# Optimization experiments

Hardware: AMD Instinct MI355X
Metric: run time of the kernel (lower is better)

## Reference

```python
import jax, jax.numpy as jnp
import numpy as np

GROUP_SIZE = 128


def dequant_rtn(qweight, scale, zero_point):
    # qweight: [O, I] int, scale/zero_point: [O, I//GROUP_SIZE]
    O, I = qweight.shape
    G = scale.shape[1]
    gs = I // G
    q = qweight.reshape(O, G, gs).astype(jnp.float32)
    zp = zero_point.astype(jnp.float32)[:, :, None]
    w = (q - zp) * scale[:, :, None]
    return w.reshape(O, I)


def setup_inputs() -> dict:
    key = jax.random.key(0)
    k1, k2, k3, k4, k5 = jax.random.split(key, 5)
    B, S, I, O = 2, 2048, 4096, 11008
    G = I // GROUP_SIZE
    x = jax.random.normal(k1, (B, S, I), dtype=jnp.float32)
    qweight = jax.random.randint(k2, (O, I), 0, 16, dtype=jnp.int32)
    scale = jax.random.uniform(k3, (O, G), dtype=jnp.float32) * 0.02 + 1e-3
    zero_point = jax.random.randint(k4, (O, G), 0, 16, dtype=jnp.int32)
    bias = jax.random.normal(k5, (O,), dtype=jnp.float32)
    return {"x": x, "qweight": qweight, "scale": scale,
            "zero_point": zero_point, "bias": bias}


def reference(x, qweight, scale, zero_point, bias):
    # weight-only path: dequant weight, then F.linear(x, w, bias)
    w = dequant_rtn(qweight, scale, zero_point)  # [O, I] fp32
    return jnp.einsum('bsi,oi->bso', x, w) + bias
```

## Files before the change

### kernel.cpp

```cpp
#include <hip/hip_runtime.h>
#include <cstdint>
#include <cstddef>

typedef __attribute__((ext_vector_type(4))) int i32x4;
typedef __bf16 bf16;
typedef __attribute__((ext_vector_type(8))) __bf16 bf16x8;
typedef __attribute__((ext_vector_type(4))) float f32x4;

#define BM 128
#define BN 128
#define BKB 128
#define GROUP_M 16
#define GM256 4
#define NXCD 8

__device__ __forceinline__ unsigned bf16_rne(float f) {
  unsigned u = __float_as_uint(f);
  unsigned r = 0x7FFFu + ((u >> 16) & 1u);
  return ((u + r) >> 16) & 0xFFFFu;
}
__device__ __forceinline__ unsigned pack2(float a, float b) {
  return bf16_rne(a) | (bf16_rne(b) << 16);
}
__device__ __forceinline__ int pack4i8(int a, int b, int c, int d) {
  return (a & 0xFF) | ((b & 0xFF) << 8) | ((c & 0xFF) << 16) | (d << 24);
}
__device__ __forceinline__ int q_i8(float v) {
  v = fminf(fmaxf(v, -127.0f), 127.0f);
  return __float2int_rn(v);
}

__global__ __launch_bounds__(256) void prep_kernel(
    const float* __restrict__ x, char* __restrict__ xq, float* __restrict__ xscale,
    int M,
    const int* __restrict__ q, const float* __restrict__ scale,
    const int* __restrict__ zp, char* __restrict__ wq, float* __restrict__ wscale,
    int K, int G) {
  __shared__ float red[4];
  const int b = blockIdx.x;
  const int tid = threadIdx.x;
  float f[16];

  if (b < M) {
    const float4* src = (const float4*)(x + (size_t)b * K);
#pragma unroll
    for (int i = 0; i < 4; ++i) {
      float4 v = src[tid + 256 * i];
      f[4 * i + 0] = v.x; f[4 * i + 1] = v.y;
      f[4 * i + 2] = v.z; f[4 * i + 3] = v.w;
    }
  } else {
    const int row = b - M;
    const int4* src = (const int4*)(q + (size_t)row * K);
    const float* srow = scale + (size_t)row * G;
    const int*   zrow = zp + (size_t)row * G;
#pragma unroll
    for (int i = 0; i < 4; ++i) {
      const int j = tid + 256 * i;
      const int g = j >> 5;
      const float s = srow[g];
      const float nzs = -s * (float)zrow[g];
      int4 qv = src[j];
      f[4 * i + 0] = fmaf((float)qv.x, s, nzs);
      f[4 * i + 1] = fmaf((float)qv.y, s, nzs);
      f[4 * i + 2] = fmaf((float)qv.z, s, nzs);
      f[4 * i + 3] = fmaf((float)qv.w, s, nzs);
    }
  }

  float m = 0.f;
#pragma unroll
  for (int j = 0; j < 16; ++j) m = fmaxf(m, fabsf(f[j]));
#pragma unroll
  for (int off = 32; off >= 1; off >>= 1) m = fmaxf(m, __shfl_xor(m, off));
  if ((tid & 63) == 0) red[tid >> 6] = m;
  __syncthreads();
  m = fmaxf(fmaxf(red[0], red[1]), fmaxf(red[2], red[3]));

  const float inv = m > 0.f ? 127.0f / m : 0.f;
  int pk[4];
#pragma unroll
  for (int i = 0; i < 4; ++i)
    pk[i] = pack4i8(q_i8(f[4 * i + 0] * inv), q_i8(f[4 * i + 1] * inv),
                    q_i8(f[4 * i + 2] * inv), q_i8(f[4 * i + 3] * inv));

  char* dst = (b < M) ? (xq + (size_t)b * K) : (wq + (size_t)(b - M) * K);
  int* dst_i32 = (int*)dst;
#pragma unroll
  for (int i = 0; i < 4; ++i) dst_i32[tid + 256 * i] = pk[i];

  if (tid == 0) {
    if (b < M) xscale[b] = m * (1.0f / 127.0f);
    else       wscale[b - M] = m * (1.0f / 127.0f);
  }
}

typedef __attribute__((address_space(1))) void gas_void;
typedef __attribute__((address_space(3))) void las_void;

__device__ __forceinline__ void load_lds16(const void* g, void* l) {
  __builtin_amdgcn_global_load_lds((gas_void*)g, (las_void*)l, 16, 0, 0);
}


#define STAGE_A_H(buf, h, ktb) do {                                           \
    load_lds16(A + abase + (size_t)(ktb) + aoff0 + (size_t)(h) * 64 * K,      \
               &Al[buf][(h) * 8192 + dw]);                                    \
    load_lds16(A + abase + (size_t)(ktb) + aoff1 + (size_t)(h) * 64 * K,      \
               &Al[buf][16384 + (h) * 8192 + dw]);                            \
  } while (0)

#define STAGE_B_H(buf, h, ktb) do {                                           \
    load_lds16(Bw + bbase + (size_t)(ktb) + boff0 + (size_t)(h) * 32 * K,     \
               &Bl[buf][(h) * 16384 + dw]);                                   \
    load_lds16(Bw + bbase + (size_t)(ktb) + boff1 + (size_t)(h) * 32 * K,     \
               &Bl[buf][(h) * 16384 + 8192 + dw]);                            \
  } while (0)

__global__ __launch_bounds__(512, 2) void gemm_i8_256(
    const char* __restrict__ A,
    const char* __restrict__ Bw,
    const float* __restrict__ ascale,
    const float* __restrict__ bscale,
    const float* __restrict__ bias,
    float* __restrict__ C,
    int M, int N, int K) {
  __shared__ __align__(16) char Al[2][256 * 128];
  __shared__ __align__(16) char Bl[2][256 * 128];
  const int tid  = threadIdx.x;
  const int wave = tid >> 6;
  const int lane = tid & 63;
  const int quad = lane >> 4;
  const int l16  = lane & 15;
  const int wq3  = wave & 3;
  const int wmb  = (wave >> 2) * 128;
  const int wnb  = wq3 * 64;

  const int nbm = M / 256, nbn = N / 256;
  const int cpx = (nbm * nbn) / NXCD;
  const int swz = ((int)blockIdx.x % NXCD) * cpx + (int)blockIdx.x / NXCD;
  const int per_group = GM256 * nbn;
  const int gid = swz / per_group;
  const int rem = swz - gid * per_group;
  int gm = nbm - gid * GM256; if (gm > GM256) gm = GM256;
  const int bm = (gid * GM256 + (rem % gm)) * 256;
  const int bn = (rem / gm) * 256;

  const int r0 = tid >> 3;
  const int kq16 = (((tid & 7) ^ (r0 & 7)) * 16);
  const size_t aoff0 = (size_t)r0 * K + kq16;
  const size_t aoff1 = aoff0 + (size_t)128 * K;
  const size_t boff0 = (size_t)((r0 >> 5) * 64 + (r0 & 31)) * K + kq16;
  const size_t boff1 = boff0 + (size_t)128 * K;
  const int dw = wave * 1024;
  const size_t abase = (size_t)bm * K;
  const size_t bbase = (size_t)bn * K;
  const int NT = K / 128;

  i32x4 acc[8][4];
#pragma unroll
  for (int i = 0; i < 8; ++i)
#pragma unroll
    for (int j = 0; j < 4; ++j)
      acc[i][j] = (i32x4){0, 0, 0, 0};

  STAGE_A_H(0, 0, 0);
  STAGE_A_H(0, 1, 0);
  STAGE_B_H(0, 0, 0);
  STAGE_B_H(0, 1, 0);
  asm volatile("s_waitcnt vmcnt(0)" ::: "memory");
  __builtin_amdgcn_s_barrier();
  __builtin_amdgcn_sched_barrier(0);

  for (int t = 0; t < NT; ++t) {
    const int cur = t & 1;
    const int nxt = cur ^ 1;
    const int kt1 = (t + 1) * 128;

    if (t + 1 < NT) {
      STAGE_A_H(nxt, 0, kt1);
      STAGE_A_H(nxt, 1, kt1);
      STAGE_B_H(nxt, 0, kt1);
      STAGE_B_H(nxt, 1, kt1);
    }

#pragma unroll
    for (int ks = 0; ks < 2; ++ks) {
      i32x4 afr[8], bfr[4];
#pragma unroll
      for (int tm = 0; tm < 8; ++tm) {
        int row = wmb + tm * 16 + l16;
        int kq  = ks * 4 + quad;
        afr[tm] = *(const i32x4*)&Al[cur][(row * 8 + (kq ^ (row & 7))) * 16];
      }
#pragma unroll
      for (int j = 0; j < 4; ++j) {
        int p  = (j >> 1) * 128 + wq3 * 32 + (j & 1) * 16 + l16;
        int kq = ks * 4 + quad;
        bfr[j] = *(const i32x4*)&Bl[cur][(p * 8 + (kq ^ (p & 7))) * 16];
      }
#pragma unroll
      for (int tm = 0; tm < 8; ++tm)
#pragma unroll
        for (int j = 0; j < 4; ++j)
          acc[tm][j] = __builtin_amdgcn_mfma_i32_16x16x64_i8(
              afr[tm], bfr[j], acc[tm][j], 0, 0, 0);
    }

    asm volatile("s_waitcnt vmcnt(0)" ::: "memory");
    __builtin_amdgcn_s_barrier();
    __builtin_amdgcn_sched_barrier(0);
  }

#pragma unroll
  for (int tn = 0; tn < 4; ++tn) {
    int col = bn + wnb + tn * 16 + l16;
    float bv = bias[col];
    float ws = bscale[col];
#pragma unroll
    for (int tm = 0; tm < 8; ++tm) {
      int row0 = bm + wmb + tm * 16 + quad * 4;
#pragma unroll
      for (int v = 0; v < 4; ++v) {
        float val = ascale[row0 + v] * ws * (float)acc[tm][tn][v] + bv;
        __builtin_nontemporal_store(val, &C[(size_t)(row0 + v) * N + col]);
      }
    }
  }
}

__global__ __launch_bounds__(256) void gemm_i8_kernel(
    const char* __restrict__ A, const char* __restrict__ Bw,
    const float* __restrict__ ascale, const float* __restrict__ bscale,
    const float* __restrict__ bias, float* __restrict__ C,
    int M, int N, int K) {
  __shared__ __align__(16) char Alds[BM * BKB];
  __shared__ __align__(16) char Blds[BN * BKB];
  const int tid  = threadIdx.x;
  const int wave = tid >> 6;
  const int lane = tid & 63;
  const int quad = lane >> 4;
  const int l16  = lane & 15;

  const int nbm = M / BM;
  const int nbn = N / BN;
  int flat = blockIdx.x;
  int per_group = GROUP_M * nbn;
  int gid = flat / per_group;
  int rem = flat - gid * per_group;
  int gm = nbm - gid * GROUP_M;
  if (gm > GROUP_M) gm = GROUP_M;
  const int bm = (gid * GROUP_M + (rem % gm)) * BM;
  const int bn = (rem / gm) * BN;

  const int wm = (wave & 1) * 64;
  const int wn = (wave >> 1) * 64;

  i32x4 acc[4][4];
#pragma unroll
  for (int i = 0; i < 4; ++i)
#pragma unroll
    for (int j = 0; j < 4; ++j)
      acc[i][j] = (i32x4){0, 0, 0, 0};

  for (int kt = 0; kt < K; kt += BKB) {
#pragma unroll
    for (int t = 0; t < 4; ++t) {
      int s0 = (wave * 4 + t) * 64;
      int s  = s0 + lane;
      int m  = s >> 3;
      int kq = (s & 7) ^ (m & 7);
      load_lds16(A  + (size_t)(bm + m) * K + kt + kq * 16, &Alds[s0 * 16]);
      load_lds16(Bw + (size_t)(bn + m) * K + kt + kq * 16, &Blds[s0 * 16]);
    }
    __syncthreads();

#pragma unroll
    for (int ks = 0; ks < 2; ++ks) {
      i32x4 af[4], bfr[4];
#pragma unroll
      for (int tm = 0; tm < 4; ++tm) {
        int m  = wm + tm * 16 + l16;
        int kq = ks * 4 + quad;
        af[tm] = *(const i32x4*)&Alds[(m * 8 + (kq ^ (m & 7))) * 16];
      }
#pragma unroll
      for (int tn = 0; tn < 4; ++tn) {
        int n  = wn + tn * 16 + l16;
        int kq = ks * 4 + quad;
        bfr[tn] = *(const i32x4*)&Blds[(n * 8 + (kq ^ (n & 7))) * 16];
      }
#pragma unroll
      for (int tm = 0; tm < 4; ++tm)
#pragma unroll
        for (int tn = 0; tn < 4; ++tn)
          acc[tm][tn] = __builtin_amdgcn_mfma_i32_16x16x64_i8(
              af[tm], bfr[tn], acc[tm][tn], 0, 0, 0);
    }
    __syncthreads();
  }

#pragma unroll
  for (int tn = 0; tn < 4; ++tn) {
    int col = bn + wn + tn * 16 + l16;
    float bv = bias[col];
    float ws = bscale[col];
#pragma unroll
    for (int tm = 0; tm < 4; ++tm) {
      int row0 = bm + wm + tm * 16 + quad * 4;
#pragma unroll
      for (int v = 0; v < 4; ++v) {
        float val = ascale[row0 + v] * ws * (float)acc[tm][tn][v] + bv;
        __builtin_nontemporal_store(val, &C[(size_t)(row0 + v) * N + col]);
      }
    }
  }
}

__global__ __launch_bounds__(256) void gemm_fused_kernel(
    const float* __restrict__ X, const int* __restrict__ Q,
    const float* __restrict__ scale, const int* __restrict__ zp,
    const float* __restrict__ bias, float* __restrict__ C,
    int M, int N, int K, int G) {
  __shared__ __align__(16) bf16 Alds[128 * 64];
  __shared__ __align__(16) bf16 Blds[128 * 64];
  const int tid  = threadIdx.x;
  const int wave = tid >> 6;
  const int lane = tid & 63;
  const int quad = lane >> 4;
  const int l16  = lane & 15;
  const int bm = blockIdx.y * 128;
  const int bn = blockIdx.x * 128;
  const int wm = (wave & 1) * 64;
  const int wn = (wave >> 1) * 64;

  f32x4 acc[4][4];
#pragma unroll
  for (int i = 0; i < 4; ++i)
#pragma unroll
    for (int j = 0; j < 4; ++j)
      acc[i][j] = (f32x4){0.f, 0.f, 0.f, 0.f};

  for (int kt = 0; kt < K; kt += 64) {
#pragma unroll
    for (int i = 0; i < 4; ++i) {
      int c = tid + i * 256;
      int m = c >> 3;
      int kq = (c & 7) ^ (m & 7);
      const float* src = X + (size_t)(bm + m) * K + kt + kq * 8;
      float4 v0 = *(const float4*)src;
      float4 v1 = *(const float4*)(src + 4);
      uint4 p;
      p.x = pack2(v0.x, v0.y); p.y = pack2(v0.z, v0.w);
      p.z = pack2(v1.x, v1.y); p.w = pack2(v1.z, v1.w);
      *(uint4*)&Alds[c * 8] = p;
    }
#pragma unroll
    for (int i = 0; i < 4; ++i) {
      int c = tid + i * 256;
      int n = c >> 3;
      int kq = (c & 7) ^ (n & 7);
      int kcol = kt + kq * 8;
      size_t row = (size_t)(bn + n);
      int g = kcol >> 7;
      float s = scale[row * G + g];
      float z = (float)zp[row * G + g];
      const int* src = Q + row * K + kcol;
      int4 q0 = *(const int4*)src;
      int4 q1 = *(const int4*)(src + 4);
      uint4 p;
      p.x = pack2(((float)q0.x - z) * s, ((float)q0.y - z) * s);
      p.y = pack2(((float)q0.z - z) * s, ((float)q0.w - z) * s);
      p.z = pack2(((float)q1.x - z) * s, ((float)q1.y - z) * s);
      p.w = pack2(((float)q1.z - z) * s, ((float)q1.w - z) * s);
      *(uint4*)&Blds[c * 8] = p;
    }
    __syncthreads();

#pragma unroll
    for (int ks = 0; ks < 2; ++ks) {
      bf16x8 af[4], bfr[4];
#pragma unroll
      for (int tm = 0; tm < 4; ++tm) {
        int m  = wm + tm * 16 + l16;
        int kq = ks * 4 + quad;
        af[tm] = *(const bf16x8*)&Alds[(m * 8 + (kq ^ (m & 7))) * 8];
      }
#pragma unroll
      for (int tn = 0; tn < 4; ++tn) {
        int n  = wn + tn * 16 + l16;
        int kq = ks * 4 + quad;
        bfr[tn] = *(const bf16x8*)&Blds[(n * 8 + (kq ^ (n & 7))) * 8];
      }
#pragma unroll
      for (int tm = 0; tm < 4; ++tm)
#pragma unroll
        for (int tn = 0; tn < 4; ++tn)
          acc[tm][tn] = __builtin_amdgcn_mfma_f32_16x16x32_bf16(
              af[tm], bfr[tn], acc[tm][tn], 0, 0, 0);
    }
    __syncthreads();
  }

#pragma unroll
  for (int tn = 0; tn < 4; ++tn) {
    int col = bn + wn + tn * 16 + l16;
    float bv = bias[col];
#pragma unroll
    for (int tm = 0; tm < 4; ++tm) {
      int row0 = bm + wm + tm * 16 + quad * 4;
#pragma unroll
      for (int v = 0; v < 4; ++v)
        C[(size_t)(row0 + v) * N + col] = acc[tm][tn][v] + bv;
    }
  }
}

extern "C" void kernel_launch(void* const* d_in, const int* in_sizes, int n_in,
                              void* d_out, int out_size, void* d_ws, size_t ws_size,
                              hipStream_t stream) {
  const float* x     = (const float*)d_in[0];
  const int*   qw    = (const int*)d_in[1];
  const float* scale = (const float*)d_in[2];
  const int*   zp    = (const int*)d_in[3];
  const float* bias  = (const float*)d_in[4];
  float* out = (float*)d_out;

  const int O = in_sizes[4];
  const int I = (int)(in_sizes[1] / O);
  const int M = (int)(in_sizes[0] / I);
  const int G = in_sizes[2] / O;
  const int K = I, N = O;

  size_t off_xq = 0;
  size_t off_xs = off_xq + (size_t)M * K;
  size_t off_wq = (off_xs + (size_t)M * 4 + 255) & ~(size_t)255;
  size_t off_ws_ = off_wq + (size_t)N * K;
  size_t need   = ((off_ws_ + (size_t)N * 4 + 255) & ~(size_t)255);

  if (ws_size >= need && K == 4096) {
    char*  xq = (char*)d_ws + off_xq;
    float* xs = (float*)((char*)d_ws + off_xs);
    char*  wq = (char*)d_ws + off_wq;
    float* wsc = (float*)((char*)d_ws + off_ws_);

    prep_kernel<<<M + N, 256, 0, stream>>>(x, xq, xs, M, qw, scale, zp, wq, wsc, K, G);

    const int nb256 = (M / 256) * (N / 256);
    if ((M % 256) == 0 && (N % 256) == 0 && (nb256 % NXCD) == 0) {
      gemm_i8_256<<<nb256, 512, 0, stream>>>(xq, wq, xs, wsc, bias, out, M, N, K);
    } else {
      int nblocks = (M / BM) * (N / BN);
      gemm_i8_kernel<<<nblocks, 256, 0, stream>>>(xq, wq, xs, wsc, bias, out, M, N, K);
    }
  } else {
    dim3 gemm_grid((unsigned)(N / 128), (unsigned)(M / 128));
    gemm_fused_kernel<<<gemm_grid, 256, 0, stream>>>(x, qw, scale, zp, bias, out,
                                                     M, N, K, G);
  }
}
```

Baseline: 562.1 us.

## Restructure int8 GEMM inner loop with explicit scheduling and analytic weight scale

The weight-quantization path now derives each row's max magnitude analytically from scale and zero-point bounds instead of reducing over dequantized values, which removes a block reduction and barrier for weight rows. The GEMM main loop loads all LDS fragments for both k-substeps up front, separates the phases with sched_barriers, and raises wave priority around the MFMA bursts. The minimum-occupancy hint of 2 blocks per CU is dropped from launch_bounds. The analytic bound can exceed the true row max, which slightly coarsens weight quantization, and holding both fragment sets raises register pressure and may reduce occupancy.

```diff
diff --git a/kernel.cpp b/kernel.cpp
--- a/kernel.cpp
+++ b/kernel.cpp
@@ -39,33 +39,45 @@
   __shared__ float red[4];
   const int b = blockIdx.x;
   const int tid = threadIdx.x;
-  float f[16];
-
-  if (b < M) {
-    const float4* src = (const float4*)(x + (size_t)b * K);
-#pragma unroll
-    for (int i = 0; i < 4; ++i) {
-      float4 v = src[tid + 256 * i];
-      f[4 * i + 0] = v.x; f[4 * i + 1] = v.y;
-      f[4 * i + 2] = v.z; f[4 * i + 3] = v.w;
-    }
-  } else {
+
+  if (b >= M) {
     const int row = b - M;
-    const int4* src = (const int4*)(q + (size_t)row * K);
     const float* srow = scale + (size_t)row * G;
     const int*   zrow = zp + (size_t)row * G;
+    const int lane = tid & 63;
+    const int g0 = lane & 31;
+    const float s0 = srow[g0];
+    const float z0 = (float)zrow[g0];
+    float bnd = s0 * fmaxf(z0, 15.0f - z0);
+#pragma unroll
+    for (int off = 16; off >= 1; off >>= 1)
+      bnd = fmaxf(bnd, __shfl_xor(bnd, off));
+    const float inv = 127.0f / bnd;
+    const int4* src = (const int4*)(q + (size_t)row * K);
+    int* dst = (int*)(wq + (size_t)row * K);
 #pragma unroll
     for (int i = 0; i < 4; ++i) {
       const int j = tid + 256 * i;
       const int g = j >> 5;
-      const float s = srow[g];
-      const float nzs = -s * (float)zrow[g];
+      const float fs = srow[g] * inv;
+      const float fo = -(float)zrow[g] * srow[g] * inv;
       int4 qv = src[j];
-      f[4 * i + 0] = fmaf((float)qv.x, s, nzs);
-      f[4 * i + 1] = fmaf((float)qv.y, s, nzs);
-      f[4 * i + 2] = fmaf((float)qv.z, s, nzs);
-      f[4 * i + 3] = fmaf((float)qv.w, s, nzs);
-    }
+      dst[j] = pack4i8(__float2int_rn(fmaf((float)qv.x, fs, fo)),
+                       __float2int_rn(fmaf((float)qv.y, fs, fo)),
+                       __float2int_rn(fmaf((float)qv.z, fs, fo)),
+                       __float2int_rn(fmaf((float)qv.w, fs, fo)));
+    }
+    if (tid == 0) wscale[row] = bnd * (1.0f / 127.0f);
+    return;
+  }
+
+  float f[16];
+  const float4* src = (const float4*)(x + (size_t)b * K);
+#pragma unroll
+  for (int i = 0; i < 4; ++i) {
+    float4 v = src[tid + 256 * i];
+    f[4 * i + 0] = v.x; f[4 * i + 1] = v.y;
+    f[4 * i + 2] = v.z; f[4 * i + 3] = v.w;
   }
 
   float m = 0.f;
@@ -84,15 +96,11 @@
     pk[i] = pack4i8(q_i8(f[4 * i + 0] * inv), q_i8(f[4 * i + 1] * inv),
                     q_i8(f[4 * i + 2] * inv), q_i8(f[4 * i + 3] * inv));
 
-  char* dst = (b < M) ? (xq + (size_t)b * K) : (wq + (size_t)(b - M) * K);
-  int* dst_i32 = (int*)dst;
+  int* dst_i32 = (int*)(xq + (size_t)b * K);
 #pragma unroll
   for (int i = 0; i < 4; ++i) dst_i32[tid + 256 * i] = pk[i];
 
-  if (tid == 0) {
-    if (b < M) xscale[b] = m * (1.0f / 127.0f);
-    else       wscale[b - M] = m * (1.0f / 127.0f);
-  }
+  if (tid == 0) xscale[b] = m * (1.0f / 127.0f);
 }
 
 typedef __attribute__((address_space(1))) void gas_void;
@@ -117,7 +125,7 @@
                &Bl[buf][(h) * 16384 + 8192 + dw]);                            \
   } while (0)
 
-__global__ __launch_bounds__(512, 2) void gemm_i8_256(
+__global__ __launch_bounds__(512) void gemm_i8_256(
     const char* __restrict__ A,
     const char* __restrict__ Bw,
     const float* __restrict__ ascale,
@@ -176,36 +184,63 @@
     const int cur = t & 1;
     const int nxt = cur ^ 1;
     const int kt1 = (t + 1) * 128;
-
-    if (t + 1 < NT) {
+    const bool s1 = (t + 1) < NT;
+
+    if (s1) {
       STAGE_A_H(nxt, 0, kt1);
       STAGE_A_H(nxt, 1, kt1);
       STAGE_B_H(nxt, 0, kt1);
       STAGE_B_H(nxt, 1, kt1);
     }
-
-#pragma unroll
-    for (int ks = 0; ks < 2; ++ks) {
-      i32x4 afr[8], bfr[4];
-#pragma unroll
-      for (int tm = 0; tm < 8; ++tm) {
-        int row = wmb + tm * 16 + l16;
-        int kq  = ks * 4 + quad;
-        afr[tm] = *(const i32x4*)&Al[cur][(row * 8 + (kq ^ (row & 7))) * 16];
-      }
-#pragma unroll
-      for (int j = 0; j < 4; ++j) {
-        int p  = (j >> 1) * 128 + wq3 * 32 + (j & 1) * 16 + l16;
-        int kq = ks * 4 + quad;
-        bfr[j] = *(const i32x4*)&Bl[cur][(p * 8 + (kq ^ (p & 7))) * 16];
-      }
-#pragma unroll
-      for (int tm = 0; tm < 8; ++tm)
-#pragma unroll
-        for (int j = 0; j < 4; ++j)
-          acc[tm][j] = __builtin_amdgcn_mfma_i32_16x16x64_i8(
-              afr[tm], bfr[j], acc[tm][j], 0, 0, 0);
-    }
+    __builtin_amdgcn_sched_barrier(0);
+
+    i32x4 afr0[8], bfr0[4], afr1[8], bfr1[4];
+#pragma unroll
+    for (int tm = 0; tm < 8; ++tm) {
+      int row = wmb + tm * 16 + l16;
+      int kq  = quad;
+      afr0[tm] = *(const i32x4*)&Al[cur][(row * 8 + (kq ^ (row & 7))) * 16];
+    }
+#pragma unroll
+    for (int j = 0; j < 4; ++j) {
+      int p  = (j >> 1) * 128 + wq3 * 32 + (j & 1) * 16 + l16;
+      int kq = quad;
+      bfr0[j] = *(const i32x4*)&Bl[cur][(p * 8 + (kq ^ (p & 7))) * 16];
+    }
+    __builtin_amdgcn_sched_barrier(0);
+
+#pragma unroll
+    for (int tm = 0; tm < 8; ++tm) {
+      int row = wmb + tm * 16 + l16;
+      int kq  = 4 + quad;
+      afr1[tm] = *(const i32x4*)&Al[cur][(row * 8 + (kq ^ (row & 7))) * 16];
+    }
+#pragma unroll
+    for (int j = 0; j < 4; ++j) {
+      int p  = (j >> 1) * 128 + wq3 * 32 + (j & 1) * 16 + l16;
+      int kq = 4 + quad;
+      bfr1[j] = *(const i32x4*)&Bl[cur][(p * 8 + (kq ^ (p & 7))) * 16];
+    }
+    __builtin_amdgcn_sched_barrier(0);
+
+    __builtin_amdgcn_s_setprio(1);
+#pragma unroll
+    for (int tm = 0; tm < 8; ++tm)
+#pragma unroll
+      for (int j = 0; j < 4; ++j)
+        acc[tm][j] = __builtin_amdgcn_mfma_i32_16x16x64_i8(
+            afr0[tm], bfr0[j], acc[tm][j], 0, 0, 0);
+    __builtin_amdgcn_s_setprio(0);
+    __builtin_amdgcn_sched_barrier(0);
+
+    __builtin_amdgcn_s_setprio(1);
+#pragma unroll
+    for (int tm = 0; tm < 8; ++tm)
+#pragma unroll
+      for (int j = 0; j < 4; ++j)
+        acc[tm][j] = __builtin_amdgcn_mfma_i32_16x16x64_i8(
+            afr1[tm], bfr1[j], acc[tm][j], 0, 0, 0);
+    __builtin_amdgcn_s_setprio(0);
 
     asm volatile("s_waitcnt vmcnt(0)" ::: "memory");
     __builtin_amdgcn_s_barrier();
```

Result: no change. 558.0 us (-0.7%).
